# Optimization experiments

Measured on AMD Instinct MI355X. Metric: run time of the kernel, lower is better.

## Reference

```python
import jax, jax.numpy as jnp
import numpy as np

EPS = 1e-5
N_HEADS = 16
D_NOPE = 128
D_ROPE = 64
D_QK = D_NOPE + D_ROPE  # 192
D_V = 128
KV_RANK = 512
SCALE = D_QK ** -0.5


def rms_norm(x, w, eps=EPS):
    return x * jax.lax.rsqrt(jnp.mean(x * x, axis=-1, keepdims=True) + eps) * w


def apply_rope(x, c, s):
    # x: [..., D_ROPE], c/s broadcastable [..., D_ROPE//2]; half-split rotation
    x0, x1 = x[..., : D_ROPE // 2], x[..., D_ROPE // 2 :]
    return jnp.concatenate([x0 * c - x1 * s, x0 * s + x1 * c], axis=-1)


def setup_inputs() -> dict:
    key = jax.random.key(0)
    ks = jax.random.split(key, 8)
    B, S, H_DIM = 2, 2048, 2048
    Q_RANK = 1536
    w = lambda k, shp: jax.random.normal(k, shp, dtype=jnp.float32) * 0.02
    # real RoPE tables: [max_seq, D_ROPE//2]
    inv_freq = 1.0 / (10000.0 ** (np.arange(0, D_ROPE, 2, dtype=np.float32) / D_ROPE))
    ang = np.arange(S, dtype=np.float32)[:, None] * inv_freq[None, :]
    return {
        "x": jax.random.normal(ks[0], (B, S, H_DIM), dtype=jnp.float32),
        "positions": jnp.arange(S, dtype=jnp.int64),
        "Wqa": w(ks[1], (H_DIM, Q_RANK)),
        "g_qa": jnp.ones((Q_RANK,), jnp.float32),
        "Wqb": w(ks[2], (Q_RANK, N_HEADS * D_QK)),
        "Wkva": w(ks[3], (H_DIM, KV_RANK + D_ROPE)),
        "g_kva": jnp.ones((KV_RANK,), jnp.float32),
        "Wkvb": w(ks[4], (KV_RANK, N_HEADS * (D_NOPE + D_V))),
        "Wo": w(ks[5], (N_HEADS * D_V, H_DIM)),
        "cos": jnp.asarray(np.cos(ang)),
        "sin": jnp.asarray(np.sin(ang)),
    }


def reference(x, positions, Wqa, g_qa, Wqb, Wkva, g_kva, Wkvb, Wo, cos, sin):
    B, S, _ = x.shape
    # Q path: low-rank down, RMSNorm, up
    q = rms_norm(x @ Wqa, g_qa) @ Wqb  # [B,S,H*D_QK]
    q = q.reshape(B, S, N_HEADS, D_QK)
    q_nope, q_rope = q[..., :D_NOPE], q[..., D_NOPE:]
    c = cos[positions]  # [S, D_ROPE//2]
    s = sin[positions]
    q_rope = apply_rope(q_rope, c[None, :, None, :], s[None, :, None, :])
    # KV path: joint down-proj, split latent / rope-key
    kv_a = x @ Wkva  # [B,S,KV_RANK+D_ROPE]
    kv_latent = rms_norm(kv_a[..., :KV_RANK], g_kva)
    k_rope = apply_rope(kv_a[..., KV_RANK:], c[None, :, :], s[None, :, :])  # [B,S,D_ROPE]
    # up-project latent to per-head k_nope and v
    kv_b = (kv_latent @ Wkvb).reshape(B, S, N_HEADS, D_NOPE + D_V)
    k_nope, v = kv_b[..., :D_NOPE], kv_b[..., D_NOPE:]
    k = jnp.concatenate(
        [k_nope, jnp.broadcast_to(k_rope[:, :, None, :], (B, S, N_HEADS, D_ROPE))], axis=-1
    )  # [B,S,H,D_QK]
    q_full = jnp.concatenate([q_nope, q_rope], axis=-1)  # [B,S,H,D_QK]
    # causal SDPA with d_qk != d_v
    scores = jnp.einsum("bqhd,bkhd->bhqk", q_full, k) * SCALE
    causal = jnp.tril(jnp.ones((S, S), dtype=bool))
    scores = jnp.where(causal[None, None, :, :], scores, -jnp.inf)
    p = jax.nn.softmax(scores, axis=-1)
    out = jnp.einsum("bhqk,bkhd->bqhd", p, v).reshape(B, S, N_HEADS * D_V)
    return out @ Wo
```

## Files before the change

### kernel.cpp

```cpp
#include <hip/hip_runtime.h>
#include <hip/hip_bf16.h>

typedef __bf16 bf16;
typedef __bf16 bf16x8 __attribute__((ext_vector_type(8)));
typedef __bf16 bf16x4 __attribute__((ext_vector_type(4)));
typedef float f32x4 __attribute__((ext_vector_type(4)));

#define B_    2
#define S_    2048
#define HD    2048
#define NH    16
#define DQK   192
#define DV    128
#define QR    1536
#define KVR   512
#define NTOK  4096
#define NKVB  4096
#define NQB   3072
#define NQKVA 2176

#define EXP2F(x) __builtin_amdgcn_exp2f(x)

static __device__ __forceinline__ void gload16(const void* g, void* l) {
  __builtin_amdgcn_global_load_lds(
      (const __attribute__((address_space(1))) void*)g,
      (__attribute__((address_space(3))) void*)l, 16, 0, 0);
}

__global__ __launch_bounds__(256) void cvt_bf16(const float* __restrict__ in,
                                                bf16* __restrict__ out, long n) {
  long i = ((long)blockIdx.x * 256 + threadIdx.x) * 4;
  if (i + 3 < n) {
    float4 v = *(const float4*)(in + i);
    bf16x4 o = {(bf16)v.x, (bf16)v.y, (bf16)v.z, (bf16)v.w};
    *(bf16x4*)(out + i) = o;
  }
}

__global__ __launch_bounds__(256) void transpose_cvt(const float* __restrict__ in,
                                                     bf16* __restrict__ out,
                                                     int R, int C, int Np) {
  __shared__ float tile[32][33];
  int c0 = blockIdx.x * 32;
  int r0 = blockIdx.y * 32;
  int tx = threadIdx.x & 31, ty = threadIdx.x >> 5;
#pragma unroll
  for (int i = 0; i < 4; ++i) {
    int r = r0 + ty + i * 8, c = c0 + tx;
    tile[ty + i * 8][tx] = (c < C) ? in[(long)r * C + c] : 0.f;
  }
  __syncthreads();
#pragma unroll
  for (int i = 0; i < 4; ++i) {
    int oc = c0 + ty + i * 8;
    if (oc < Np) out[(long)oc * R + r0 + tx] = (bf16)tile[tx][ty + i * 8];
  }
}

#define GEMM_CORE(A, Bt, K)                                                    \
  __shared__ bf16 As[128 * 64];                                                \
  __shared__ bf16 Bs[128 * 64];                                                \
  const int t = threadIdx.x;                                                   \
  const int l = t & 63;                                                        \
  const int w = t >> 6;                                                        \
  const int m0 = blockIdx.y * 128;                                             \
  const int n0 = blockIdx.x * 128;                                             \
  const int wr = (w >> 1) * 64;                                                \
  const int wc = (w & 1) * 64;                                                 \
  const int lr = l & 15;                                                       \
  const int lg = l >> 4;                                                       \
  f32x4 acc[4][4] = {};                                                        \
  for (int k0 = 0; k0 < (K); k0 += 64) {                                       \
    __syncthreads();                                                           \
    _Pragma("unroll")                                                          \
    for (int j = 0; j < 4; ++j) {                                              \
      int s = j * 256 + t;                                                     \
      int row = s >> 3, sc = s & 7;                                            \
      int c = sc ^ (row & 7);                                                  \
      gload16((A) + (long)(m0 + row) * (K) + k0 + c * 8,                       \
              As + (j * 256 + w * 64) * 8);                                    \
      gload16((Bt) + (long)(n0 + row) * (K) + k0 + c * 8,                      \
              Bs + (j * 256 + w * 64) * 8);                                    \
    }                                                                          \
    __syncthreads();                                                           \
    _Pragma("unroll")                                                          \
    for (int kh = 0; kh < 2; ++kh) {                                           \
      bf16x8 af[4], bfr[4];                                                    \
      _Pragma("unroll")                                                        \
      for (int m = 0; m < 4; ++m) {                                            \
        int row = wr + m * 16 + lr;                                            \
        af[m] = *(const bf16x8*)(As + row * 64 + (((kh * 4 + lg) ^ (row & 7)) << 3)); \
      }                                                                        \
      _Pragma("unroll")                                                        \
      for (int n = 0; n < 4; ++n) {                                            \
        int row = wc + n * 16 + lr;                                            \
        bfr[n] = *(const bf16x8*)(Bs + row * 64 + (((kh * 4 + lg) ^ (row & 7)) << 3)); \
      }                                                                        \
      _Pragma("unroll")                                                        \
      for (int m = 0; m < 4; ++m)                                              \
        _Pragma("unroll")                                                      \
        for (int n = 0; n < 4; ++n)                                            \
          acc[m][n] = __builtin_amdgcn_mfma_f32_16x16x32_bf16(af[m], bfr[n], acc[m][n], 0, 0, 0); \
    }                                                                          \
  }

template <typename CT>
__global__ __launch_bounds__(256) void gemm_bf16(const bf16* __restrict__ A,
                                                 const bf16* __restrict__ Bt,
                                                 CT* __restrict__ C,
                                                 int M, int N, int K) {
  GEMM_CORE(A, Bt, K)
#pragma unroll
  for (int m = 0; m < 4; ++m)
#pragma unroll
    for (int n = 0; n < 4; ++n)
#pragma unroll
      for (int v = 0; v < 4; ++v) {
        int row = m0 + wr + m * 16 + lg * 4 + v;
        int col = n0 + wc + n * 16 + lr;
        C[(long)row * N + col] = (CT)acc[m][n][v];
      }
}

__global__ __launch_bounds__(256) void gemm_qf(const bf16* __restrict__ A,
                                               const bf16* __restrict__ Bt,
                                               const int* __restrict__ pos,
                                               const float* __restrict__ cosT,
                                               const float* __restrict__ sinT,
                                               bf16* __restrict__ q_bhsd) {
  const float SCALE = 0.07216878364870323f * 1.4426950408889634f;
  GEMM_CORE(A, Bt, QR)
  int c0 = n0 + wc;
  int h = c0 / 192;
  int part = c0 - h * 192;
#pragma unroll
  for (int m = 0; m < 4; ++m)
#pragma unroll
    for (int v = 0; v < 4; ++v) {
      int row = m0 + wr + m * 16 + lg * 4 + v;
      int b = row >> 11, s = row & (S_ - 1);
      long base = ((long)(b * NH + h) * S_ + s) * DQK;
      if (part < 128) {
#pragma unroll
        for (int n = 0; n < 4; ++n)
          q_bhsd[base + part + n * 16 + lr] = (bf16)(acc[m][n][v] * SCALE);
      } else {
        int p = pos[s] & (S_ - 1);
        float c_lo = cosT[p * 32 + lr],      s_lo = sinT[p * 32 + lr];
        float c_hi = cosT[p * 32 + 16 + lr], s_hi = sinT[p * 32 + 16 + lr];
        float o0 = acc[m][0][v] * c_lo - acc[m][2][v] * s_lo;
        float o1 = acc[m][1][v] * c_hi - acc[m][3][v] * s_hi;
        float o2 = acc[m][0][v] * s_lo + acc[m][2][v] * c_lo;
        float o3 = acc[m][1][v] * s_hi + acc[m][3][v] * c_hi;
        q_bhsd[base + 128 + lr] = (bf16)(o0 * SCALE);
        q_bhsd[base + 144 + lr] = (bf16)(o1 * SCALE);
        q_bhsd[base + 160 + lr] = (bf16)(o2 * SCALE);
        q_bhsd[base + 176 + lr] = (bf16)(o3 * SCALE);
      }
    }
}

__global__ __launch_bounds__(256) void gemm_kvb(const bf16* __restrict__ A,
                                                const bf16* __restrict__ Bt,
                                                bf16* __restrict__ k_bhsd,
                                                bf16* __restrict__ v_rows) {
  GEMM_CORE(A, Bt, KVR)
  int c0 = n0 + wc;
  int h = c0 >> 8;
  int dbase = c0 & 64;
  bool vpart = (c0 >> 7) & 1;
#pragma unroll
  for (int m = 0; m < 4; ++m)
#pragma unroll
    for (int v = 0; v < 4; ++v) {
      int row = m0 + wr + m * 16 + lg * 4 + v;
      int b = row >> 11, s = row & (S_ - 1);
      if (!vpart) {
        long base = ((long)(b * NH + h) * S_ + s) * DQK + dbase;
#pragma unroll
        for (int n = 0; n < 4; ++n)
          k_bhsd[base + n * 16 + lr] = (bf16)acc[m][n][v];
      } else {
        long base = (long)row * 2048 + h * 128 + dbase;
#pragma unroll
        for (int n = 0; n < 4; ++n)
          v_rows[base + n * 16 + lr] = (bf16)acc[m][n][v];
      }
    }
}

__global__ __launch_bounds__(256) void norm_prep(const bf16* __restrict__ xa,
                                                 const float* __restrict__ g_qa,
                                                 const float* __restrict__ g_kva,
                                                 const int* __restrict__ pos,
                                                 const float* __restrict__ cosT,
                                                 const float* __restrict__ sinT,
                                                 bf16* __restrict__ q_n,
                                                 bf16* __restrict__ kv_l,
                                                 bf16* __restrict__ k_bhsd) {
  int row = blockIdx.x;
  int t = threadIdx.x;
  int b = row >> 11, s = row & (S_ - 1);
  const bf16* xr = xa + (long)row * NQKVA;
  __shared__ float red[3];
  __shared__ bf16 rope_s[64];
  float vf[8];
  if (t < 192) {
    bf16x8 vv = *(const bf16x8*)(xr + t * 8);
    float ss = 0.f;
#pragma unroll
    for (int e = 0; e < 8; ++e) { vf[e] = (float)vv[e]; ss += vf[e] * vf[e]; }
#pragma unroll
    for (int m = 1; m < 64; m <<= 1) ss += __shfl_xor(ss, m);
    if ((t & 63) == 0) red[t >> 6] = ss;
  } else {
    int tt = t - 192;
    const bf16* xl = xr + QR;
    bf16x8 vv = *(const bf16x8*)(xl + tt * 8);
    float ss = 0.f;
#pragma unroll
    for (int e = 0; e < 8; ++e) { vf[e] = (float)vv[e]; ss += vf[e] * vf[e]; }
#pragma unroll
    for (int m = 1; m < 64; m <<= 1) ss += __shfl_xor(ss, m);
    float rs = rsqrtf(ss / KVR + 1e-5f);
    bf16x8 o;
#pragma unroll
    for (int e = 0; e < 8; ++e) o[e] = (bf16)(vf[e] * rs * g_kva[tt * 8 + e]);
    *(bf16x8*)(kv_l + (long)row * KVR + tt * 8) = o;
    if (tt < 32) {
      int p = pos[s] & (S_ - 1);
      float c = cosT[p * 32 + tt], sn = sinT[p * 32 + tt];
      float x0 = (float)xl[512 + tt], x1 = (float)xl[544 + tt];
      rope_s[tt] = (bf16)(x0 * c - x1 * sn);
      rope_s[32 + tt] = (bf16)(x0 * sn + x1 * c);
    }
  }
  __syncthreads();
  if (t < 192) {
    float ss = red[0] + red[1] + red[2];
    float rs = rsqrtf(ss / QR + 1e-5f);
    bf16x8 o;
#pragma unroll
    for (int e = 0; e < 8; ++e) o[e] = (bf16)(vf[e] * rs * g_qa[t * 8 + e]);
    *(bf16x8*)(q_n + (long)row * QR + t * 8) = o;
  } else {
    int tt = t - 192;
    bf16x8 rv = *(const bf16x8*)&rope_s[(tt & 7) * 8];
    long base0 = ((long)(b * NH + (tt >> 3)) * S_ + s) * DQK + 128 + (tt & 7) * 8;
    long base1 = ((long)(b * NH + 8 + (tt >> 3)) * S_ + s) * DQK + 128 + (tt & 7) * 8;
    *(bf16x8*)(k_bhsd + base0) = rv;
    *(bf16x8*)(k_bhsd + base1) = rv;
  }
}

__global__ __launch_bounds__(256) void v_trans(const bf16* __restrict__ v_rows,
                                               bf16* __restrict__ v_t) {
  __shared__ bf16 tile[32][33];
  int st = blockIdx.x, dt = blockIdx.y, bh = blockIdx.z;
  int b = bh >> 4, h = bh & 15;
  int tx = threadIdx.x & 31, ty = threadIdx.x >> 5;
#pragma unroll
  for (int i = 0; i < 4; ++i) {
    int s = st * 32 + ty + i * 8, d = dt * 32 + tx;
    tile[ty + i * 8][tx] = v_rows[((long)(b * S_ + s)) * 2048 + h * 128 + d];
  }
  __syncthreads();
#pragma unroll
  for (int i = 0; i < 4; ++i) {
    int d = dt * 32 + ty + i * 8, s = st * 32 + tx;
    v_t[((long)bh * DV + d) * S_ + s] = tile[tx][ty + i * 8];
  }
}

#define QBLK 64
#define KVB  64
#define DVP  144
__global__ __launch_bounds__(256) void flash2(const bf16* __restrict__ q_bhsd,
                                              const bf16* __restrict__ k_bhsd,
                                              const bf16* __restrict__ v_t,
                                              bf16* __restrict__ att) {
  __shared__ bf16 Ks[KVB * DQK];
  __shared__ bf16 Vs[DVP * KVB];
  __shared__ bf16 Ps[4][16 * 72];
  int bid = blockIdx.x;
  int bh = bid & 31;
  int qt = 31 - (bid >> 5);
  int b = bh >> 4, h = bh & 15;
  int q0 = qt * QBLK;
  int t = threadIdx.x;
  int w = t >> 6, l = t & 63;
  int lr = l & 15, lg = l >> 4;
  int qw = q0 + w * 16;

  const bf16* Qb = q_bhsd + (long)bh * S_ * DQK;
  const bf16* Kb = k_bhsd + (long)bh * S_ * DQK;
  const bf16* Vb = v_t + (long)bh * DV * S_;

  if (t < 128) {
    int rr = 128 + (t >> 3), cc = (t & 7) * 8;
    bf16 val = (bf16)((rr == 128) ? 1.0f : 0.0f);
    bf16x8 vvv = {val, val, val, val, val, val, val, val};
    *(bf16x8*)(Vs + rr * KVB + cc) = vvv;
  }

  bf16x8 qf[6];
#pragma unroll
  for (int t6 = 0; t6 < 6; ++t6)
    qf[t6] = *(const bf16x8*)(Qb + (long)(qw + lr) * DQK + t6 * 32 + lg * 8);

  f32x4 oacc[9] = {};
  float mrow[4] = {-1e30f, -1e30f, -1e30f, -1e30f};
  const int lr7 = lr & 7;

  int nkt = qt + 1;
  for (int kt = 0; kt < nkt; ++kt) {
    int k0 = kt * KVB;
    __syncthreads();
#pragma unroll
    for (int j = 0; j < 6; ++j) {
      int s = j * 256 + t;
      int r = s / 24, c1 = s - r * 24;
      int c = c1 ^ (r & 7);
      gload16(Kb + (long)(k0 + r) * DQK + c * 8, Ks + (j * 256 + w * 64) * 8);
    }
#pragma unroll
    for (int j = 0; j < 4; ++j) {
      int s = j * 256 + t;
      int d = s >> 3, c1 = s & 7;
      int c = c1 ^ (d & 7);
      gload16(Vb + (long)d * S_ + k0 + c * 8, Vs + (j * 256 + w * 64) * 8);
    }
    __syncthreads();
    if (k0 > qw + 15) continue;

    f32x4 sacc[4] = {};
#pragma unroll
    for (int n = 0; n < 4; ++n) {
      int rk = n * 16 + lr;
#pragma unroll
      for (int t6 = 0; t6 < 6; ++t6) {
        bf16x8 kf = *(const bf16x8*)(Ks + rk * DQK + (((t6 * 4 + lg) ^ lr7) << 3));
        sacc[n] = __builtin_amdgcn_mfma_f32_16x16x32_bf16(qf[t6], kf, sacc[n], 0, 0, 0);
      }
    }
    if (k0 + KVB - 1 > qw) {
#pragma unroll
      for (int n = 0; n < 4; ++n)
#pragma unroll
        for (int v = 0; v < 4; ++v) {
          int r = lg * 4 + v, c = n * 16 + lr;
          if (k0 + c > qw + r) sacc[n][v] = -1e30f;
        }
    }
    float corr[4], p[4][4];
#pragma unroll
    for (int v = 0; v < 4; ++v) {
      float mv = fmaxf(fmaxf(sacc[0][v], sacc[1][v]), fmaxf(sacc[2][v], sacc[3][v]));
#pragma unroll
      for (int msk = 1; msk < 16; msk <<= 1) mv = fmaxf(mv, __shfl_xor(mv, msk));
      float mt = fmaxf(mrow[v], mv);
      corr[v] = EXP2F(mrow[v] - mt);
#pragma unroll
      for (int n = 0; n < 4; ++n) p[n][v] = EXP2F(sacc[n][v] - mt);
      mrow[v] = mt;
    }
#pragma unroll
    for (int dn = 0; dn < 9; ++dn)
#pragma unroll
      for (int v = 0; v < 4; ++v) oacc[dn][v] *= corr[v];
#pragma unroll
    for (int v = 0; v < 4; ++v)
#pragma unroll
      for (int n = 0; n < 4; ++n)
        Ps[w][(lg * 4 + v) * 72 + n * 16 + lr] = (bf16)p[n][v];
#pragma unroll
    for (int kc = 0; kc < 2; ++kc) {
      bf16x8 pf = *(const bf16x8*)(Ps[w] + lr * 72 + kc * 32 + lg * 8);
#pragma unroll
      for (int dn = 0; dn < 9; ++dn) {
        int d = dn * 16 + lr;
        bf16x8 vf = *(const bf16x8*)(Vs + d * KVB + (((kc * 4 + lg) ^ lr7) << 3));
        oacc[dn] = __builtin_amdgcn_mfma_f32_16x16x32_bf16(pf, vf, oacc[dn], 0, 0, 0);
      }
    }
  }
  float rl[4];
#pragma unroll
  for (int v = 0; v < 4; ++v) {
    float lv = __shfl(oacc[8][v], lg * 16);
    rl[v] = 1.0f / lv;
  }
#pragma unroll
  for (int dn = 0; dn < 8; ++dn)
#pragma unroll
    for (int v = 0; v < 4; ++v) {
      int r = lg * 4 + v;
      float o = oacc[dn][v] * rl[v];
      att[((long)(b * S_ + qw + r)) * 2048 + h * 128 + dn * 16 + lr] = (bf16)o;
    }
}

extern "C" void kernel_launch(void* const* d_in, const int* in_sizes, int n_in,
                              void* d_out, int out_size, void* d_ws, size_t ws_size,
                              hipStream_t stream) {
  const float* x        = (const float*)d_in[0];
  const int* pos        = (const int*)d_in[1];
  const float* Wqa      = (const float*)d_in[2];
  const float* g_qa     = (const float*)d_in[3];
  const float* Wqb      = (const float*)d_in[4];
  const float* Wkva     = (const float*)d_in[5];
  const float* g_kva    = (const float*)d_in[6];
  const float* Wkvb     = (const float*)d_in[7];
  const float* Wo       = (const float*)d_in[8];
  const float* cosT     = (const float*)d_in[9];
  const float* sinT     = (const float*)d_in[10];
  float* out            = (float*)d_out;

  size_t off = 0;
  char* wsp = (char*)d_ws;
  auto alloc = [&](size_t n) { void* p = wsp + off; off += (n + 255) & ~(size_t)255; return p; };
  bf16*  Wqa_t  = (bf16*) alloc((size_t)QR * HD * 2);
  bf16*  Wkva_t = (bf16*) alloc((size_t)640 * HD * 2);
  bf16*  Wqb_t  = (bf16*) alloc((size_t)NQB * QR * 2);
  bf16*  Wkvb_t = (bf16*) alloc((size_t)NKVB * KVR * 2);
  bf16*  Wo_t   = (bf16*) alloc((size_t)HD * HD * 2);
  bf16*  x_bf   = (bf16*) alloc((size_t)NTOK * HD * 2);
  bf16*  q_bhsd = (bf16*) alloc((size_t)B_ * NH * S_ * DQK * 2);
  bf16*  k_bhsd = (bf16*) alloc((size_t)B_ * NH * S_ * DQK * 2);
  bf16*  v_rows = (bf16*) alloc((size_t)NTOK * 2048 * 2);
  bf16*  v_t    = (bf16*) alloc((size_t)B_ * NH * DV * S_ * 2);
  bf16*  att    = (bf16*) alloc((size_t)NTOK * 2048 * 2);
  char*  T      = (char*) alloc((size_t)33554432);
  bf16*  xa  = (bf16*)T;
  bf16*  q_n = (bf16*)(T + 18874368);
  bf16*  kv_l = (bf16*)(T + 18874368 + 12582912);
  if (ws_size < off) return;

  cvt_bf16<<<(NTOK * HD / 4 + 255) / 256, 256, 0, stream>>>(x, x_bf, (long)NTOK * HD);
  transpose_cvt<<<dim3(QR / 32, HD / 32), 256, 0, stream>>>(Wqa, Wqa_t, HD, QR, QR);
  transpose_cvt<<<dim3(640 / 32, HD / 32), 256, 0, stream>>>(Wkva, Wkva_t, HD, 576, 640);
  transpose_cvt<<<dim3(NQB / 32, QR / 32), 256, 0, stream>>>(Wqb, Wqb_t, QR, NQB, NQB);
  transpose_cvt<<<dim3(NKVB / 32, KVR / 32), 256, 0, stream>>>(Wkvb, Wkvb_t, KVR, NKVB, NKVB);
  transpose_cvt<<<dim3(HD / 32, HD / 32), 256, 0, stream>>>(Wo, Wo_t, HD, HD, HD);
  gemm_bf16<bf16><<<dim3(NQKVA / 128, NTOK / 128), 256, 0, stream>>>(x_bf, Wqa_t, xa, NTOK, NQKVA, HD);
  norm_prep<<<NTOK, 256, 0, stream>>>(xa, g_qa, g_kva, pos, cosT, sinT, q_n, kv_l, k_bhsd);
  gemm_qf<<<dim3(NQB / 128, NTOK / 128), 256, 0, stream>>>(q_n, Wqb_t, pos, cosT, sinT, q_bhsd);
  gemm_kvb<<<dim3(NKVB / 128, NTOK / 128), 256, 0, stream>>>(kv_l, Wkvb_t, k_bhsd, v_rows);
  v_trans<<<dim3(S_ / 32, DV / 32, B_ * NH), 256, 0, stream>>>(v_rows, v_t);
  flash2<<<1024, 256, 0, stream>>>(q_bhsd, k_bhsd, v_t, att);
  gemm_bf16<float><<<dim3(HD / 128, NTOK / 128), 256, 0, stream>>>(att, Wo_t, out, NTOK, HD, HD);
}
```

Before: 334.8 us.

## Replace GEMM core with triple-buffered 256x128 ping-pong pipeline and MFMA priority

Replaces the single-buffered 128x128 GEMM core with a 256x128 tile run by 512 threads. It uses a triple-buffered LDS ring that prefetches two k-tiles ahead, with explicit vmcnt/lgkmcnt waits and barriers. MFMA phases are wrapped in setprio, and global loads are interleaved between the two half-N compute phases. The attention kernel also gets setprio around its MFMA loops. The aim is to hide global-load latency behind matrix math and raise MFMA utilization, at the cost of much more LDS (about 144KB) and fewer resident blocks.

```diff
diff --git a/kernel.cpp b/kernel.cpp
--- a/kernel.cpp
+++ b/kernel.cpp
@@ -57,101 +57,142 @@
   }
 }
 
-#define GEMM_CORE(A, Bt, K)                                                    \
-  __shared__ bf16 As[128 * 64];                                                \
-  __shared__ bf16 Bs[128 * 64];                                                \
+#define G2P_CORE(A, Bt, K)                                                     \
+  __shared__ bf16 La[3][256 * 64];                                             \
+  __shared__ bf16 Lb[3][128 * 64];                                             \
   const int t = threadIdx.x;                                                   \
-  const int l = t & 63;                                                        \
-  const int w = t >> 6;                                                        \
-  const int m0 = blockIdx.y * 128;                                             \
-  const int n0 = blockIdx.x * 128;                                             \
-  const int wr = (w >> 1) * 64;                                                \
-  const int wc = (w & 1) * 64;                                                 \
-  const int lr = l & 15;                                                       \
-  const int lg = l >> 4;                                                       \
+  const int w = t >> 6, l = t & 63;                                            \
+  const int lr = l & 15, lg = l >> 4;                                          \
+  const int wm = w >> 1, wn = w & 1;                                           \
+  const int m0 = blockIdx.y * 256, n0 = blockIdx.x * 128;                      \
+  const int NT = (K) >> 6;                                                     \
+  const int tr = t >> 3, sc = t & 7;                                           \
   f32x4 acc[4][4] = {};                                                        \
-  for (int k0 = 0; k0 < (K); k0 += 64) {                                       \
-    __syncthreads();                                                           \
+        \
+  auto stA = [&](int kt, int r) {                                              \
+    int row = r * 64 + tr;                                                     \
+    int c = sc ^ (row & 7);                                                    \
+    gload16((A) + (long)(m0 + row) * (K) + kt * 64 + c * 8,                    \
+            &La[kt % 3][(r * 512 + w * 64) * 8]);                              \
+  };                                                                           \
+  auto stB = [&](int kt, int r) {                                              \
+    int row = r * 64 + tr;                                                     \
+    int c = sc ^ (row & 7);                                                    \
+    gload16((Bt) + (long)(n0 + row) * (K) + kt * 64 + c * 8,                   \
+            &Lb[kt % 3][(r * 512 + w * 64) * 8]);                              \
+  };                                                                           \
+                             \
+  stA(0, 0); stA(0, 1); stA(0, 2); stA(0, 3); stB(0, 0); stB(0, 1);            \
+  stA(1, 0); stA(1, 1); stA(1, 2); stA(1, 3); stB(1, 0); stB(1, 1);            \
+  for (int kt = 0; kt < NT; ++kt) {                                            \
+    const bf16* Ab = &La[kt % 3][0];                                           \
+    const bf16* Bb = &Lb[kt % 3][0];                                           \
+    bool more = (kt + 2) < NT;                                                 \
+    \
+    if (kt == NT - 1) { asm volatile("s_waitcnt vmcnt(0)" ::: "memory"); }     \
+    else              { asm volatile("s_waitcnt vmcnt(6)" ::: "memory"); }     \
+    __builtin_amdgcn_s_barrier();                                              \
+    bf16x8 af[4][2], bf0[2][2];                                                \
     _Pragma("unroll")                                                          \
-    for (int j = 0; j < 4; ++j) {                                              \
-      int s = j * 256 + t;                                                     \
-      int row = s >> 3, sc = s & 7;                                            \
-      int c = sc ^ (row & 7);                                                  \
-      gload16((A) + (long)(m0 + row) * (K) + k0 + c * 8,                       \
-              As + (j * 256 + w * 64) * 8);                                    \
-      gload16((Bt) + (long)(n0 + row) * (K) + k0 + c * 8,                      \
-              Bs + (j * 256 + w * 64) * 8);                                    \
+    for (int mi = 0; mi < 4; ++mi) {                                           \
+      int row = wm * 64 + mi * 16 + lr;                                        \
+      _Pragma("unroll")                                                        \
+      for (int kh = 0; kh < 2; ++kh)                                           \
+        af[mi][kh] = *(const bf16x8*)(Ab + row * 64 + (((kh * 4 + lg) ^ (row & 7)) << 3)); \
     }                                                                          \
-    __syncthreads();                                                           \
     _Pragma("unroll")                                                          \
-    for (int kh = 0; kh < 2; ++kh) {                                           \
-      bf16x8 af[4], bfr[4];                                                    \
+    for (int ni = 0; ni < 2; ++ni) {                                           \
+      int row = wn * 64 + ni * 16 + lr;                                        \
       _Pragma("unroll")                                                        \
-      for (int m = 0; m < 4; ++m) {                                            \
-        int row = wr + m * 16 + lr;                                            \
-        af[m] = *(const bf16x8*)(As + row * 64 + (((kh * 4 + lg) ^ (row & 7)) << 3)); \
-      }                                                                        \
+      for (int kh = 0; kh < 2; ++kh)                                           \
+        bf0[ni][kh] = *(const bf16x8*)(Bb + row * 64 + (((kh * 4 + lg) ^ (row & 7)) << 3)); \
+    }                                                                          \
+    if (more) { stA(kt + 2, 0); stA(kt + 2, 1); stA(kt + 2, 2); }              \
+    asm volatile("s_waitcnt lgkmcnt(0)" ::: "memory");                         \
+    __builtin_amdgcn_sched_barrier(0);                                         \
+    __builtin_amdgcn_s_setprio(1);                                             \
+    _Pragma("unroll")                                                          \
+    for (int mi = 0; mi < 4; ++mi)                                             \
       _Pragma("unroll")                                                        \
-      for (int n = 0; n < 4; ++n) {                                            \
-        int row = wc + n * 16 + lr;                                            \
-        bfr[n] = *(const bf16x8*)(Bs + row * 64 + (((kh * 4 + lg) ^ (row & 7)) << 3)); \
-      }                                                                        \
+      for (int ni = 0; ni < 2; ++ni)                                           \
+        _Pragma("unroll")                                                      \
+        for (int kh = 0; kh < 2; ++kh)                                         \
+          acc[mi][ni] = __builtin_amdgcn_mfma_f32_16x16x32_bf16(af[mi][kh], bf0[ni][kh], acc[mi][ni], 0, 0, 0); \
+    __builtin_amdgcn_s_setprio(0);                                             \
+    __builtin_amdgcn_s_barrier();                                              \
+             \
+    bf16x8 bf1[2][2];                                                          \
+    _Pragma("unroll")                                                          \
+    for (int ni = 0; ni < 2; ++ni) {                                           \
+      int row = wn * 64 + (ni + 2) * 16 + lr;                                  \
       _Pragma("unroll")                                                        \
-      for (int m = 0; m < 4; ++m)                                              \
+      for (int kh = 0; kh < 2; ++kh)                                           \
+        bf1[ni][kh] = *(const bf16x8*)(Bb + row * 64 + (((kh * 4 + lg) ^ (row & 7)) << 3)); \
+    }                                                                          \
+    if (more) { stA(kt + 2, 3); stB(kt + 2, 0); stB(kt + 2, 1); }              \
+    __builtin_amdgcn_s_barrier();                                              \
+    asm volatile("s_waitcnt lgkmcnt(0)" ::: "memory");                         \
+    __builtin_amdgcn_sched_barrier(0);                                         \
+    __builtin_amdgcn_s_setprio(1);                                             \
+    _Pragma("unroll")                                                          \
+    for (int mi = 0; mi < 4; ++mi)                                             \
+      _Pragma("unroll")                                                        \
+      for (int ni = 0; ni < 2; ++ni)                                           \
         _Pragma("unroll")                                                      \
-        for (int n = 0; n < 4; ++n)                                            \
-          acc[m][n] = __builtin_amdgcn_mfma_f32_16x16x32_bf16(af[m], bfr[n], acc[m][n], 0, 0, 0); \
-    }                                                                          \
+        for (int kh = 0; kh < 2; ++kh)                                         \
+          acc[mi][ni + 2] = __builtin_amdgcn_mfma_f32_16x16x32_bf16(af[mi][kh], bf1[ni][kh], acc[mi][ni + 2], 0, 0, 0); \
+    __builtin_amdgcn_s_setprio(0);                                             \
+    __builtin_amdgcn_s_barrier();                                              \
   }
 
 template <typename CT>
-__global__ __launch_bounds__(256) void gemm_bf16(const bf16* __restrict__ A,
+__global__ __launch_bounds__(512) void gemm2p(const bf16* __restrict__ A,
+                                              const bf16* __restrict__ Bt,
+                                              CT* __restrict__ C,
+                                              int M, int N, int K) {
+  G2P_CORE(A, Bt, K)
+#pragma unroll
+  for (int mi = 0; mi < 4; ++mi)
+#pragma unroll
+    for (int ni = 0; ni < 4; ++ni)
+#pragma unroll
+      for (int vv = 0; vv < 4; ++vv) {
+        int row = m0 + wm * 64 + mi * 16 + lg * 4 + vv;
+        int col = n0 + wn * 64 + ni * 16 + lr;
+        C[(long)row * N + col] = (CT)acc[mi][ni][vv];
+      }
+}
+
+__global__ __launch_bounds__(512) void gemm2p_qf(const bf16* __restrict__ A,
                                                  const bf16* __restrict__ Bt,
-                                                 CT* __restrict__ C,
-                                                 int M, int N, int K) {
-  GEMM_CORE(A, Bt, K)
-#pragma unroll
-  for (int m = 0; m < 4; ++m)
-#pragma unroll
-    for (int n = 0; n < 4; ++n)
-#pragma unroll
-      for (int v = 0; v < 4; ++v) {
-        int row = m0 + wr + m * 16 + lg * 4 + v;
-        int col = n0 + wc + n * 16 + lr;
-        C[(long)row * N + col] = (CT)acc[m][n][v];
-      }
-}
-
-__global__ __launch_bounds__(256) void gemm_qf(const bf16* __restrict__ A,
-                                               const bf16* __restrict__ Bt,
-                                               const int* __restrict__ pos,
-                                               const float* __restrict__ cosT,
-                                               const float* __restrict__ sinT,
-                                               bf16* __restrict__ q_bhsd) {
+                                                 const int* __restrict__ pos,
+                                                 const float* __restrict__ cosT,
+                                                 const float* __restrict__ sinT,
+                                                 bf16* __restrict__ q_bhsd) {
   const float SCALE = 0.07216878364870323f * 1.4426950408889634f;
-  GEMM_CORE(A, Bt, QR)
-  int c0 = n0 + wc;
+  G2P_CORE(A, Bt, QR)
+  int c0 = n0 + wn * 64;
   int h = c0 / 192;
   int part = c0 - h * 192;
 #pragma unroll
-  for (int m = 0; m < 4; ++m)
-#pragma unroll
-    for (int v = 0; v < 4; ++v) {
-      int row = m0 + wr + m * 16 + lg * 4 + v;
+  for (int mi = 0; mi < 4; ++mi)
+#pragma unroll
+    for (int vv = 0; vv < 4; ++vv) {
+      int row = m0 + wm * 64 + mi * 16 + lg * 4 + vv;
       int b = row >> 11, s = row & (S_ - 1);
       long base = ((long)(b * NH + h) * S_ + s) * DQK;
       if (part < 128) {
 #pragma unroll
-        for (int n = 0; n < 4; ++n)
-          q_bhsd[base + part + n * 16 + lr] = (bf16)(acc[m][n][v] * SCALE);
+        for (int ni = 0; ni < 4; ++ni)
+          q_bhsd[base + part + ni * 16 + lr] = (bf16)(acc[mi][ni][vv] * SCALE);
       } else {
         int p = pos[s] & (S_ - 1);
         float c_lo = cosT[p * 32 + lr],      s_lo = sinT[p * 32 + lr];
         float c_hi = cosT[p * 32 + 16 + lr], s_hi = sinT[p * 32 + 16 + lr];
-        float o0 = acc[m][0][v] * c_lo - acc[m][2][v] * s_lo;
-        float o1 = acc[m][1][v] * c_hi - acc[m][3][v] * s_hi;
-        float o2 = acc[m][0][v] * s_lo + acc[m][2][v] * c_lo;
-        float o3 = acc[m][1][v] * s_hi + acc[m][3][v] * c_hi;
+        float o0 = acc[mi][0][vv] * c_lo - acc[mi][2][vv] * s_lo;
+        float o1 = acc[mi][1][vv] * c_hi - acc[mi][3][vv] * s_hi;
+        float o2 = acc[mi][0][vv] * s_lo + acc[mi][2][vv] * c_lo;
+        float o3 = acc[mi][1][vv] * s_hi + acc[mi][3][vv] * c_hi;
         q_bhsd[base + 128 + lr] = (bf16)(o0 * SCALE);
         q_bhsd[base + 144 + lr] = (bf16)(o1 * SCALE);
         q_bhsd[base + 160 + lr] = (bf16)(o2 * SCALE);
@@ -160,31 +201,31 @@
     }
 }
 
-__global__ __launch_bounds__(256) void gemm_kvb(const bf16* __restrict__ A,
-                                                const bf16* __restrict__ Bt,
-                                                bf16* __restrict__ k_bhsd,
-                                                bf16* __restrict__ v_rows) {
-  GEMM_CORE(A, Bt, KVR)
-  int c0 = n0 + wc;
+__global__ __launch_bounds__(512) void gemm2p_kvb(const bf16* __restrict__ A,
+                                                  const bf16* __restrict__ Bt,
+                                                  bf16* __restrict__ k_bhsd,
+                                                  bf16* __restrict__ v_rows) {
+  G2P_CORE(A, Bt, KVR)
+  int c0 = n0 + wn * 64;
   int h = c0 >> 8;
   int dbase = c0 & 64;
   bool vpart = (c0 >> 7) & 1;
 #pragma unroll
-  for (int m = 0; m < 4; ++m)
-#pragma unroll
-    for (int v = 0; v < 4; ++v) {
-      int row = m0 + wr + m * 16 + lg * 4 + v;
+  for (int mi = 0; mi < 4; ++mi)
+#pragma unroll
+    for (int vv = 0; vv < 4; ++vv) {
+      int row = m0 + wm * 64 + mi * 16 + lg * 4 + vv;
       int b = row >> 11, s = row & (S_ - 1);
       if (!vpart) {
         long base = ((long)(b * NH + h) * S_ + s) * DQK + dbase;
 #pragma unroll
-        for (int n = 0; n < 4; ++n)
-          k_bhsd[base + n * 16 + lr] = (bf16)acc[m][n][v];
+        for (int ni = 0; ni < 4; ++ni)
+          k_bhsd[base + ni * 16 + lr] = (bf16)acc[mi][ni][vv];
       } else {
         long base = (long)row * 2048 + h * 128 + dbase;
 #pragma unroll
-        for (int n = 0; n < 4; ++n)
-          v_rows[base + n * 16 + lr] = (bf16)acc[m][n][v];
+        for (int ni = 0; ni < 4; ++ni)
+          v_rows[base + ni * 16 + lr] = (bf16)acc[mi][ni][vv];
       }
     }
 }
@@ -334,6 +375,7 @@
     if (k0 > qw + 15) continue;
 
     f32x4 sacc[4] = {};
+    __builtin_amdgcn_s_setprio(1);
 #pragma unroll
     for (int n = 0; n < 4; ++n) {
       int rk = n * 16 + lr;
@@ -343,6 +385,7 @@
         sacc[n] = __builtin_amdgcn_mfma_f32_16x16x32_bf16(qf[t6], kf, sacc[n], 0, 0, 0);
       }
     }
+    __builtin_amdgcn_s_setprio(0);
     if (k0 + KVB - 1 > qw) {
 #pragma unroll
       for (int n = 0; n < 4; ++n)
@@ -373,6 +416,7 @@
 #pragma unroll
       for (int n = 0; n < 4; ++n)
         Ps[w][(lg * 4 + v) * 72 + n * 16 + lr] = (bf16)p[n][v];
+    __builtin_amdgcn_s_setprio(1);
 #pragma unroll
     for (int kc = 0; kc < 2; ++kc) {
       bf16x8 pf = *(const bf16x8*)(Ps[w] + lr * 72 + kc * 32 + lg * 8);
@@ -383,6 +427,7 @@
         oacc[dn] = __builtin_amdgcn_mfma_f32_16x16x32_bf16(pf, vf, oacc[dn], 0, 0, 0);
       }
     }
+    __builtin_amdgcn_s_setprio(0);
   }
   float rl[4];
 #pragma unroll
@@ -442,11 +487,11 @@
   transpose_cvt<<<dim3(NQB / 32, QR / 32), 256, 0, stream>>>(Wqb, Wqb_t, QR, NQB, NQB);
   transpose_cvt<<<dim3(NKVB / 32, KVR / 32), 256, 0, stream>>>(Wkvb, Wkvb_t, KVR, NKVB, NKVB);
   transpose_cvt<<<dim3(HD / 32, HD / 32), 256, 0, stream>>>(Wo, Wo_t, HD, HD, HD);
-  gemm_bf16<bf16><<<dim3(NQKVA / 128, NTOK / 128), 256, 0, stream>>>(x_bf, Wqa_t, xa, NTOK, NQKVA, HD);
+  gemm2p<bf16><<<dim3(NQKVA / 128, NTOK / 256), 512, 0, stream>>>(x_bf, Wqa_t, xa, NTOK, NQKVA, HD);
   norm_prep<<<NTOK, 256, 0, stream>>>(xa, g_qa, g_kva, pos, cosT, sinT, q_n, kv_l, k_bhsd);
-  gemm_qf<<<dim3(NQB / 128, NTOK / 128), 256, 0, stream>>>(q_n, Wqb_t, pos, cosT, sinT, q_bhsd);
-  gemm_kvb<<<dim3(NKVB / 128, NTOK / 128), 256, 0, stream>>>(kv_l, Wkvb_t, k_bhsd, v_rows);
+  gemm2p_qf<<<dim3(NQB / 128, NTOK / 256), 512, 0, stream>>>(q_n, Wqb_t, pos, cosT, sinT, q_bhsd);
+  gemm2p_kvb<<<dim3(NKVB / 128, NTOK / 256), 512, 0, stream>>>(kv_l, Wkvb_t, k_bhsd, v_rows);
   v_trans<<<dim3(S_ / 32, DV / 32, B_ * NH), 256, 0, stream>>>(v_rows, v_t);
   flash2<<<1024, 256, 0, stream>>>(q_bhsd, k_bhsd, v_t, att);
-  gemm_bf16<float><<<dim3(HD / 128, NTOK / 128), 256, 0, stream>>>(att, Wo_t, out, NTOK, HD, HD);
-}
+  gemm2p<float><<<dim3(HD / 128, NTOK / 256), 512, 0, stream>>>(att, Wo_t, out, NTOK, HD, HD);
+}
```

New measurement: 344.6 us. 1.03x slower.
